# Performance work log

Measured on AMD Instinct MI355X. Metric: run time of the kernel, lower is better.

The kernel has to match this reference:

```python
import jax, jax.numpy as jnp
import numpy as np

CHUNK = 32
H = 4

def silu(x):
    return x * jax.nn.sigmoid(x)

def l2norm(x):
    return x * jax.lax.rsqrt(jnp.sum(x * x, -1, keepdims=True) + 1e-6)

def dwconv_causal(x_cl, w):
    # x_cl: (b, C, L), w: (C, k) depthwise causal conv (cross-correlation, left pad k-1)
    k = w.shape[1]
    xp = jnp.pad(x_cl, ((0, 0), (0, 0), (k - 1, 0)))
    return jax.lax.conv_general_dilated(xp, w[:, None, :], (1,), 'VALID',
        dimension_numbers=('NCH', 'OIH', 'NCH'), feature_group_count=x_cl.shape[1])

def short_conv_silu(x_bld, w):
    y = dwconv_causal(jnp.swapaxes(x_bld, 1, 2), w)
    return silu(jnp.swapaxes(y, 1, 2))

def delta_rule_chunkwise(q, k, v, beta, chunk=CHUNK):
    # q,k: (b,h,L,dk)  v: (b,h,L,dv)  beta: (b,h,L)
    b, h, L, dk = q.shape
    dv = v.shape[-1]
    pad = (-L) % chunk
    if pad:
        q, k, v = (jnp.pad(t, ((0, 0), (0, 0), (0, pad), (0, 0))) for t in (q, k, v))
        beta = jnp.pad(beta, ((0, 0), (0, 0), (0, pad)))
    n = (L + pad) // chunk
    q = l2norm(q)
    k = l2norm(k)
    v = v * beta[..., None]
    kb = k * beta[..., None]
    ch = lambda x: x.reshape(b, h, n, chunk, x.shape[-1])
    qc, kc, vc, kbc = map(ch, (q, k, v, kb))
    idx = jnp.arange(chunk)
    strict_lower = (idx[:, None] > idx[None, :]).astype(q.dtype)
    incl_lower = (idx[:, None] >= idx[None, :]).astype(q.dtype)
    # forward substitution to invert (I - tril(beta K K^T, -1)) per chunk
    attn = -jnp.einsum('bhncd,bhned->bhnce', kbc, kc) * strict_lower
    for i in range(1, chunk):
        upd = jnp.einsum('...j,...ji->...i', attn[..., i, :], attn[..., :, :i])
        attn = attn.at[..., i, :i].add(upd)
    attn = attn + jnp.eye(chunk, dtype=q.dtype)
    u = attn @ vc          # (b,h,n,c,dv)
    w = attn @ kbc         # (b,h,n,c,dk)
    xs = tuple(jnp.moveaxis(t, 2, 0) for t in (qc, kc, u, w))
    S0 = jnp.zeros((b, h, dk, dv), q.dtype)
    def step(S, x):
        qi, ki, ui, wi = x
        a_loc = jnp.einsum('bhcd,bhed->bhce', qi, ki) * incl_lower
        ui = ui - wi @ S
        oi = qi @ S + a_loc @ ui
        S = S + jnp.einsum('bhcd,bhcv->bhdv', ki, ui)
        return S, oi
    S, o = jax.lax.scan(step, S0, xs)
    o = jnp.moveaxis(o, 0, 2).reshape(b, h, n * chunk, dv)[:, :, :L]
    return o, S

def multiscale_conv(v, ms_w3, ms_w15, ms_w31, kernel_mix_w, channel_mixer_w):
    # v: (b,l,h,d)
    b, l, h, d = v.shape
    x = jnp.swapaxes(v.reshape(b, l, h * d), 1, 2)  # (b, h*d, l)
    outs = [dwconv_causal(x, w) for w in (ms_w3, ms_w15, ms_w31)]
    y = jnp.concatenate(outs, axis=1)               # (b, 3*h*d, l)
    # faithful to torch rearrange 'b (h kd) l -> b l h kd' on the concat layout
    y = y.reshape(b, h, 3 * d, l).transpose(0, 3, 1, 2)  # (b,l,h,3d)
    y = y @ kernel_mix_w                            # (b,l,h,d)
    y = (y.reshape(b, l, h * d) @ channel_mixer_w).reshape(b, l, h, d)
    return y

def _forward(hidden_states, Wq, Wk, Wv, Wb, conv_q_w, conv_k_w, conv_v_w,
             ms_w3, ms_w15, ms_w31, kernel_mix_w, channel_mixer_w,
             fusion_w1, fusion_b1, fusion_w2, fusion_b2, o_norm_w, Wo):
    b, L, D = hidden_states.shape
    h = H
    dk = Wq.shape[1] // h
    dv = Wv.shape[1] // h
    q = short_conv_silu(hidden_states @ Wq, conv_q_w).reshape(b, L, h, dk)
    k = short_conv_silu(hidden_states @ Wk, conv_k_w).reshape(b, L, h, dk)
    v = short_conv_silu(hidden_states @ Wv, conv_v_w).reshape(b, L, h, dv)
    v_direct = v
    beta = jax.nn.sigmoid(hidden_states @ Wb)  # (b,L,h)
    tr = lambda x: jnp.swapaxes(x, 1, 2)
    delta_out, _S = delta_rule_chunkwise(tr(q), tr(k), tr(v), tr(beta))
    delta_out = jnp.swapaxes(delta_out, 1, 2)  # (b,L,h,dv)
    ms_out = multiscale_conv(v_direct, ms_w3, ms_w15, ms_w31, kernel_mix_w, channel_mixer_w)
    bn = lambda x: jnp.mean(jnp.abs(x), -1)    # (b,L,h)
    gate_features = jnp.concatenate([hidden_states, bn(ms_out), bn(delta_out), bn(v_direct)], -1)
    hdn = jax.nn.gelu(gate_features @ fusion_w1 + fusion_b1, approximate=False)
    logits = (hdn @ fusion_w2 + fusion_b2).reshape(b, L, h, 3)
    wts = jax.nn.softmax(logits, -1)
    o = wts[..., 0:1] * ms_out + wts[..., 1:2] * delta_out + wts[..., 2:3] * v_direct
    o = o * jax.lax.rsqrt(jnp.mean(o * o, -1, keepdims=True) + 1e-5) * o_norm_w  # RMSNorm
    return o.reshape(b, L, h * dv) @ Wo

def setup_inputs() -> dict:
    B, L, D = 4, 2048, 1024
    h, d = H, D // H
    key = jax.random.key(0)
    ks = jax.random.split(key, 20)
    nrm = lambda k, shp, s: (jax.random.normal(k, shp, dtype=jnp.float32) * s)
    inp = {
        'hidden_states': nrm(ks[0], (B, L, D), 1.0),
        'Wq': nrm(ks[1], (D, D), D ** -0.5),
        'Wk': nrm(ks[2], (D, D), D ** -0.5),
        'Wv': nrm(ks[3], (D, D), D ** -0.5),
        'Wb': nrm(ks[4], (D, h), D ** -0.5),
        'conv_q_w': nrm(ks[5], (D, 4), 0.3),
        'conv_k_w': nrm(ks[6], (D, 4), 0.3),
        'conv_v_w': nrm(ks[7], (D, 4), 0.3),
        'ms_w3': nrm(ks[8], (D, 3), 0.02),
        'ms_w15': nrm(ks[9], (D, 15), 0.02),
        'ms_w31': nrm(ks[10], (D, 31), 0.02),
        'kernel_mix_w': nrm(ks[11], (3 * d, d), (3 * d) ** -0.5),
        'channel_mixer_w': nrm(ks[12], (D, D), D ** -0.5),
        'fusion_w1': nrm(ks[13], (D + 3 * h, 2 * D), (D + 3 * h) ** -0.5),
        'fusion_b1': jnp.zeros((2 * D,), jnp.float32),
        'fusion_w2': nrm(ks[14], (2 * D, 3 * h), (2 * D) ** -0.5),
        'fusion_b2': jnp.concatenate([jnp.zeros((2 * h,), jnp.float32), jnp.ones((h,), jnp.float32)]),
        'o_norm_w': jnp.ones((d,), jnp.float32),
        'Wo': nrm(ks[15], (D, D), D ** -0.5),
    }
    return inp

def reference(hidden_states, Wq, Wk, Wv, Wb, conv_q_w, conv_k_w, conv_v_w,
              ms_w3, ms_w15, ms_w31, kernel_mix_w, channel_mixer_w,
              fusion_w1, fusion_b1, fusion_w2, fusion_b2, o_norm_w, Wo):
    return _forward(hidden_states, Wq, Wk, Wv, Wb, conv_q_w, conv_k_w, conv_v_w,
                    ms_w3, ms_w15, ms_w31, kernel_mix_w, channel_mixer_w,
                    fusion_w1, fusion_b1, fusion_w2, fusion_b2, o_norm_w, Wo)
```

## Files before the change

### kernel.cpp

```cpp
#include <hip/hip_runtime.h>
#include <math.h>


typedef __attribute__((ext_vector_type(8))) __bf16 bf16x8;
typedef __attribute__((ext_vector_type(4))) float f32x4;

__device__ inline ushort f2bf(float f) {
    union { float f; unsigned u; } x; x.f = f;
    unsigned u = x.u;
    u += 0x7fffu + ((u >> 16) & 1u);
    return (ushort)(u >> 16);
}
__device__ inline float bf2f(ushort h) {
    union { unsigned u; float f; } x; x.u = ((unsigned)h) << 16;
    return x.f;
}
__device__ inline float ldf(float v) { return v; }
__device__ inline float ldf(ushort v) { return bf2f(v); }

template<int EPI>
__global__ __launch_bounds__(256) void gemm_mfma(
    const ushort* __restrict__ A, const ushort* __restrict__ BT,
    const float* __restrict__ bias, const float* __restrict__ extA,
    const float* __restrict__ extB, void* __restrict__ Cout,
    int M, int N, int K)
{
    __shared__ ushort As[2][128 * 32];
    __shared__ ushort Bs[2][128 * 32];
    __shared__ float bns[(EPI >= 2) ? 128 * 13 : 1];
    __shared__ float exb[(EPI >= 2) ? 12 * 128 : 1];
    const int tid = threadIdx.x;
    const int row0 = blockIdx.y * 128, col0 = blockIdx.x * 128;
    const int lane = tid & 63, wave = tid >> 6;
    const int wr = (wave >> 1) * 64, wc = (wave & 1) * 64;

    if (EPI >= 2) {
        for (int e = tid; e < 128 * 12; e += 256)
            bns[(e / 12) * 13 + (e % 12)] = extA[(long)(row0 + e / 12) * 12 + e % 12];
        for (int e = tid; e < 12 * 128; e += 256)
            exb[e] = extB[(long)(e >> 7) * N + col0 + (e & 127)];
    }

    f32x4 acc[4][4];
    #pragma unroll
    for (int m = 0; m < 4; ++m)
        #pragma unroll
        for (int n = 0; n < 4; ++n) {
            acc[m][n][0] = 0.f; acc[m][n][1] = 0.f;
            acc[m][n][2] = 0.f; acc[m][n][3] = 0.f;
        }

    const int rA = lane & 15;
    const int ko = (lane >> 4) * 8;
    const int srow = tid >> 2;
    const int skk = (tid & 3) * 8;

    for (int k0 = 0; k0 < K; k0 += 64) {
        #pragma unroll
        for (int hf = 0; hf < 2; ++hf) {
            #pragma unroll
            for (int i = 0; i < 2; ++i) {
                const long ga = (long)(row0 + i * 64 + srow) * K + k0 + hf * 32 + skk;
                __builtin_amdgcn_global_load_lds(
                    (const __attribute__((address_space(1))) void*)(A + ga),
                    (__attribute__((address_space(3))) void*)(&As[hf][0] + i * 2048 + wave * 512),
                    16, 0, 0);
                const long gb = (long)(col0 + i * 64 + srow) * K + k0 + hf * 32 + skk;
                __builtin_amdgcn_global_load_lds(
                    (const __attribute__((address_space(1))) void*)(BT + gb),
                    (__attribute__((address_space(3))) void*)(&Bs[hf][0] + i * 2048 + wave * 512),
                    16, 0, 0);
            }
        }
        __syncthreads();
        #pragma unroll
        for (int hf = 0; hf < 2; ++hf) {
            bf16x8 af[4], bfr[4];
            #pragma unroll
            for (int m = 0; m < 4; ++m)
                af[m] = *(const bf16x8*)(&As[hf][0] + (wr + m * 16 + rA) * 32 + ko);
            #pragma unroll
            for (int n = 0; n < 4; ++n)
                bfr[n] = *(const bf16x8*)(&Bs[hf][0] + (wc + n * 16 + rA) * 32 + ko);
            #pragma unroll
            for (int m = 0; m < 4; ++m)
                #pragma unroll
                for (int n = 0; n < 4; ++n)
                    acc[m][n] = __builtin_amdgcn_mfma_f32_16x16x32_bf16(af[m], bfr[n], acc[m][n], 0, 0, 0);
        }
        __syncthreads();
    }

    const int crow = (lane >> 4) * 4;
    const int ccol = lane & 15;
    #pragma unroll
    for (int m = 0; m < 4; ++m) {
        #pragma unroll
        for (int n = 0; n < 4; ++n) {
            #pragma unroll
            for (int r = 0; r < 4; ++r) {
                const int rl = wr + m * 16 + crow + r;
                const int cl = wc + n * 16 + ccol;
                float vv = acc[m][n][r];
                if (EPI >= 2) {
                    vv += bias[col0 + cl];
                    #pragma unroll
                    for (int j = 0; j < 12; ++j) vv += bns[rl * 13 + j] * exb[j * 128 + cl];
                    vv = 0.5f * vv * (1.f + erff(vv * 0.70710678118654752f));
                }
                const long off = (long)(row0 + rl) * N + col0 + cl;
                if (EPI == 0) ((float*)Cout)[off] = vv;
                else ((ushort*)Cout)[off] = f2bf(vv);
            }
        }
    }
}

__global__ __launch_bounds__(256) void transpose_cast(const float* __restrict__ W,
    ushort* __restrict__ WT, int K, int N)
{
    __shared__ float t[32][33];
    const int k0 = blockIdx.y * 32, n0 = blockIdx.x * 32;
    const int c = threadIdx.x & 31, r8 = threadIdx.x >> 5;
    #pragma unroll
    for (int rr = 0; rr < 4; ++rr) {
        const int r = r8 + rr * 8;
        t[r][c] = W[(long)(k0 + r) * N + n0 + c];
    }
    __syncthreads();
    #pragma unroll
    for (int rr = 0; rr < 4; ++rr) {
        const int r = r8 + rr * 8;
        WT[(long)(n0 + r) * K + k0 + c] = f2bf(t[c][r]);
    }
}

__global__ __launch_bounds__(256) void cast_bf16(const float* __restrict__ x,
    ushort* __restrict__ y)
{
    const long i = ((long)blockIdx.x * 256 + threadIdx.x) * 4;
    const float4 v = *(const float4*)(x + i);
    ushort4 o;
    o.x = f2bf(v.x); o.y = f2bf(v.y); o.z = f2bf(v.z); o.w = f2bf(v.w);
    *(ushort4*)(y + i) = o;
}

template<int NOUT, int MODE, typename TA>
__global__ __launch_bounds__(256) void gemm_smallN(const TA* __restrict__ A,
    const float* __restrict__ Bm, const float* __restrict__ bias,
    float* __restrict__ Cm, int K)
{
    __shared__ float part[4][NOUT];
    __shared__ float sm[NOUT];
    const int m = blockIdx.x, tid = threadIdx.x;
    const TA* ar = A + (long)m * K;
    float acc[NOUT];
    #pragma unroll
    for (int j = 0; j < NOUT; ++j) acc[j] = 0.f;
    for (int k = tid; k < K; k += 256) {
        const float a = ldf(ar[k]);
        #pragma unroll
        for (int j = 0; j < NOUT; ++j) acc[j] += a * Bm[(long)k * NOUT + j];
    }
    #pragma unroll
    for (int j = 0; j < NOUT; ++j)
        for (int off = 32; off > 0; off >>= 1) acc[j] += __shfl_down(acc[j], off);
    const int wid = tid >> 6, lane = tid & 63;
    if (lane == 0) {
        #pragma unroll
        for (int j = 0; j < NOUT; ++j) part[wid][j] = acc[j];
    }
    __syncthreads();
    if (tid < NOUT) {
        float s = part[0][tid] + part[1][tid] + part[2][tid] + part[3][tid];
        if (MODE == 0) {
            Cm[(long)m * NOUT + tid] = 1.f / (1.f + expf(-s));
        } else {
            sm[tid] = s + bias[tid];
        }
    }
    if (MODE == 1) {
        __syncthreads();
        if (tid < NOUT) {
            const int hh = tid / 3, r = tid - hh * 3;
            const float a0 = sm[hh * 3], a1 = sm[hh * 3 + 1], a2 = sm[hh * 3 + 2];
            const float mx = fmaxf(a0, fmaxf(a1, a2));
            const float e0 = expf(a0 - mx), e1 = expf(a1 - mx), e2 = expf(a2 - mx);
            const float mine = (r == 0) ? e0 : ((r == 1) ? e1 : e2);
            Cm[(long)m * NOUT + tid] = mine / (e0 + e1 + e2);
        }
    }
}

__global__ __launch_bounds__(256) void conv4_silu(const ushort* __restrict__ x,
    const float* __restrict__ wc, float* __restrict__ y)
{
    const long idx = (long)blockIdx.x * 256 + threadIdx.x;
    const int c = (int)(idx & 1023);
    const long bl = idx >> 10;
    const int l = (int)(bl & 2047);
    const ushort* xp = x + bl * 1024 + c;
    const float* wp = wc + c * 4;
    float s = 0.f;
    #pragma unroll
    for (int t = 0; t < 4; ++t) {
        const int ll = l - 3 + t;
        if (ll >= 0) s += bf2f(xp[(long)(ll - l) * 1024]) * wp[t];
    }
    y[idx] = s / (1.f + expf(-s));
}

__global__ __launch_bounds__(256) void conv4_silu_l2norm(const ushort* __restrict__ x,
    const float* __restrict__ wc, ushort* __restrict__ y)
{
    const int bl = blockIdx.x, tid = threadIdx.x;
    const int l = bl & 2047;
    const int c0 = tid * 4;
    const ushort* xp = x + (long)bl * 1024 + c0;
    float s[4] = {0.f, 0.f, 0.f, 0.f};
    #pragma unroll
    for (int t = 0; t < 4; ++t) {
        const int ll = l - 3 + t;
        if (ll >= 0) {
            const ushort4 xv = *(const ushort4*)(xp + (long)(ll - l) * 1024);
            s[0] += bf2f(xv.x) * wc[(c0 + 0) * 4 + t];
            s[1] += bf2f(xv.y) * wc[(c0 + 1) * 4 + t];
            s[2] += bf2f(xv.z) * wc[(c0 + 2) * 4 + t];
            s[3] += bf2f(xv.w) * wc[(c0 + 3) * 4 + t];
        }
    }
    #pragma unroll
    for (int i = 0; i < 4; ++i) s[i] = s[i] / (1.f + expf(-s[i]));
    float ss = s[0] * s[0] + s[1] * s[1] + s[2] * s[2] + s[3] * s[3];
    for (int off = 32; off > 0; off >>= 1) ss += __shfl_down(ss, off);
    ss = __shfl(ss, 0);
    const float inv = rsqrtf(ss + 1e-6f);
    ushort4 o;
    o.x = f2bf(s[0] * inv); o.y = f2bf(s[1] * inv);
    o.z = f2bf(s[2] * inv); o.w = f2bf(s[3] * inv);
    *(ushort4*)(y + (long)bl * 1024 + c0) = o;
}

__global__ __launch_bounds__(256) void chunk_prep(
    const ushort* __restrict__ qn, const ushort* __restrict__ kn,
    const float* __restrict__ v, const float* __restrict__ beta,
    float* __restrict__ u, ushort* __restrict__ w16,
    ushort* __restrict__ kT16, ushort* __restrict__ al16)
{
    __shared__ __align__(16) ushort kn16[32 * 264];
    __shared__ __align__(16) ushort kb16[32 * 264];
    __shared__ __align__(16) float  vb[32 * 260];
    __shared__ float Ms[32 * 33];
    __shared__ float Rs[32 * 33];
    __shared__ float bet[32];
    const int blk = blockIdx.x;
    const int n = blk & 63;
    const int bh = blk >> 6;
    const int h = bh & 3;
    const int b = bh >> 2;
    const int tid = threadIdx.x;
    const long lbase = (long)b * 2048 + n * 32;

    if (tid < 32) bet[tid] = beta[(lbase + tid) * 4 + h];
    __syncthreads();

    #pragma unroll
    for (int it = 0; it < 4; ++it) {
        const int e2 = tid + it * 256;
        const int c = e2 >> 5, d8 = (e2 & 31) * 8;
        const uint4 kv = *(const uint4*)(kn + (lbase + c) * 1024 + h * 256 + d8);
        *(uint4*)&kn16[c * 264 + d8] = kv;
        const float bc = bet[c];
        uint4 kb;
        kb.x = (uint)f2bf(bf2f((ushort)(kv.x & 0xffffu)) * bc) |
               ((uint)f2bf(bf2f((ushort)(kv.x >> 16)) * bc) << 16);
        kb.y = (uint)f2bf(bf2f((ushort)(kv.y & 0xffffu)) * bc) |
               ((uint)f2bf(bf2f((ushort)(kv.y >> 16)) * bc) << 16);
        kb.z = (uint)f2bf(bf2f((ushort)(kv.z & 0xffffu)) * bc) |
               ((uint)f2bf(bf2f((ushort)(kv.z >> 16)) * bc) << 16);
        kb.w = (uint)f2bf(bf2f((ushort)(kv.w & 0xffffu)) * bc) |
               ((uint)f2bf(bf2f((ushort)(kv.w >> 16)) * bc) << 16);
        *(uint4*)&kb16[c * 264 + d8] = kb;
    }
    #pragma unroll
    for (int it = 0; it < 8; ++it) {
        const int e2 = tid + it * 256;
        const int c = e2 >> 6, d4 = (e2 & 63) * 4;
        float4 vv = *(const float4*)(v + (lbase + c) * 1024 + h * 256 + d4);
        const float bc = bet[c];
        vv.x *= bc; vv.y *= bc; vv.z *= bc; vv.w *= bc;
        *(float4*)&vb[c * 260 + d4] = vv;
    }
    __syncthreads();

    for (int e = tid; e < 8192; e += 256)
        kT16[(long)blk * 8192 + e] = kn16[(e & 31) * 264 + (e >> 5)];

    const int lane = tid & 63, wave = tid >> 6;
    const int wr2 = (wave >> 1) * 16, wc2 = (wave & 1) * 16;
    const int rA = lane & 15, ko = (lane >> 4) * 8;
    {
        f32x4 accM, accA;
        accM[0] = 0.f; accM[1] = 0.f; accM[2] = 0.f; accM[3] = 0.f;
        accA[0] = 0.f; accA[1] = 0.f; accA[2] = 0.f; accA[3] = 0.f;
        const ushort* qrow = qn + (lbase + wr2 + rA) * 1024 + h * 256 + ko;
        #pragma unroll
        for (int ks = 0; ks < 8; ++ks) {
            const bf16x8 bfK = *(const bf16x8*)&kn16[(wc2 + rA) * 264 + ks * 32 + ko];
            const bf16x8 afM = *(const bf16x8*)&kb16[(wr2 + rA) * 264 + ks * 32 + ko];
            accM = __builtin_amdgcn_mfma_f32_16x16x32_bf16(afM, bfK, accM, 0, 0, 0);
            const bf16x8 afQ = *(const bf16x8*)(qrow + ks * 32);
            accA = __builtin_amdgcn_mfma_f32_16x16x32_bf16(afQ, bfK, accA, 0, 0, 0);
        }
        const int ccol = lane & 15, crow = (lane >> 4) * 4;
        #pragma unroll
        for (int r = 0; r < 4; ++r) {
            const int i = wr2 + crow + r, j = wc2 + ccol;
            const float mv = (i > j) ? -accM[r] : 0.f;
            Ms[i * 33 + j] = mv;
            Rs[i * 33 + j] = mv + ((i == j) ? 1.f : 0.f);
            al16[(long)blk * 1024 + i * 32 + j] = f2bf((i >= j) ? accA[r] : 0.f);
        }
    }
    __syncthreads();

    const int j = tid & 31, i0 = tid >> 5;
    for (int it = 0; it < 4; ++it) {
        float p4[4] = {0.f, 0.f, 0.f, 0.f};
        for (int kk = 0; kk < 32; ++kk) {
            const float pb = Ms[kk * 33 + j];
            #pragma unroll
            for (int ii = 0; ii < 4; ++ii) p4[ii] += Ms[(i0 + 8 * ii) * 33 + kk] * pb;
        }
        __syncthreads();
        #pragma unroll
        for (int ii = 0; ii < 4; ++ii) Ms[(i0 + 8 * ii) * 33 + j] = p4[ii];
        __syncthreads();
        float r4[4] = {0.f, 0.f, 0.f, 0.f};
        for (int kk = 0; kk < 32; ++kk) {
            const float pb = Ms[kk * 33 + j];
            #pragma unroll
            for (int ii = 0; ii < 4; ++ii) r4[ii] += Rs[(i0 + 8 * ii) * 33 + kk] * pb;
        }
        __syncthreads();
        #pragma unroll
        for (int ii = 0; ii < 4; ++ii) Rs[(i0 + 8 * ii) * 33 + j] += r4[ii];
        __syncthreads();
    }

    {
        const int dd = tid;
        float accU[32], accW[32];
        #pragma unroll
        for (int r = 0; r < 32; ++r) { accU[r] = 0.f; accW[r] = 0.f; }
        for (int kk = 0; kk < 32; ++kk) {
            const float vv = vb[kk * 260 + dd];
            const float bb = bf2f(kb16[kk * 264 + dd]);
            #pragma unroll
            for (int r = 0; r < 32; ++r) {
                const float rr = Rs[r * 33 + kk];
                accU[r] += rr * vv;
                accW[r] += rr * bb;
            }
        }
        const long base = (long)blk * 32;
        #pragma unroll
        for (int r = 0; r < 32; ++r) {
            u  [(base + r) * 256 + dd] = accU[r];
            w16[(base + r) * 256 + dd] = f2bf(accW[r]);
        }
    }
}

__global__ __launch_bounds__(64, 1) void delta_scan_mfma(
    const ushort* __restrict__ q16, const ushort* __restrict__ kT16,
    const ushort* __restrict__ w16, const float* __restrict__ u,
    const ushort* __restrict__ al16, float* __restrict__ dt)
{
    __shared__ __align__(16) ushort Sb[16 * 264];
    __shared__ __align__(16) ushort Ub[16 * 40];
    const int blk = blockIdx.x;
    const int bh = blk & 15;
    const int sl = blk >> 4;
    const int h = bh & 3;
    const int b = bh >> 2;
    const int v0 = sl * 16;
    const int lane = threadIdx.x;
    const int col = lane & 15;
    const int grp = lane >> 4;

    const ushort* wp  = w16  + ((long)bh * 64 * 32 + col) * 256 + grp * 8;
    const ushort* qp  = q16  + ((long)b * 2048 + col) * 1024 + h * 256 + grp * 8;
    const ushort* kp  = kT16 + ((long)bh * 64 * 256 + col) * 32 + grp * 8;
    const ushort* ap  = al16 + ((long)bh * 64 * 32 + col) * 32 + grp * 8;
    const float*  Ug  = u    + ((long)bh * 64 * 32 + grp * 4) * 256 + v0 + col;
    float*        dp  = dt   + ((long)b * 2048 + grp * 4) * 1024 + h * 256 + v0 + col;

    f32x4 S[16];
    #pragma unroll
    for (int t = 0; t < 16; ++t) { S[t][0] = 0.f; S[t][1] = 0.f; S[t][2] = 0.f; S[t][3] = 0.f; }

    bf16x8 wf[2][8], qf[2][8], kf[16], alf[2], sf[8];
    float upre[8];

    #pragma unroll
    for (int kb = 0; kb < 8; ++kb)
        #pragma unroll
        for (int e = 0; e < 8; ++e) sf[kb][e] = (__bf16)0.f;

    #pragma unroll
    for (int rt = 0; rt < 2; ++rt)
        #pragma unroll
        for (int kb = 0; kb < 8; ++kb) {
            wf[rt][kb] = *(const bf16x8*)(wp + rt * 4096 + kb * 32);
            qf[rt][kb] = *(const bf16x8*)(qp + (long)rt * 16384 + kb * 32);
        }
    #pragma unroll
    for (int t = 0; t < 16; ++t) kf[t] = *(const bf16x8*)(kp + t * 512);
    alf[0] = *(const bf16x8*)(ap);
    alf[1] = *(const bf16x8*)(ap + 512);
    #pragma unroll
    for (int rt = 0; rt < 2; ++rt)
        #pragma unroll
        for (int r = 0; r < 4; ++r)
            upre[rt * 4 + r] = Ug[rt * 4096 + r * 256];

    for (int n = 0; n < 64; ++n) {
        f32x4 up[2];
        #pragma unroll
        for (int rt = 0; rt < 2; ++rt) {
            f32x4 a; a[0] = 0.f; a[1] = 0.f; a[2] = 0.f; a[3] = 0.f;
            #pragma unroll
            for (int kb = 0; kb < 8; ++kb)
                a = __builtin_amdgcn_mfma_f32_16x16x32_bf16(wf[rt][kb], sf[kb], a, 0, 0, 0);
            #pragma unroll
            for (int r = 0; r < 4; ++r)
                up[rt][r] = upre[rt * 4 + r] - a[r];
        }
        if (n < 63) {
            #pragma unroll
            for (int rt = 0; rt < 2; ++rt)
                #pragma unroll
                for (int kb = 0; kb < 8; ++kb)
                    wf[rt][kb] = *(const bf16x8*)(wp + (long)(n + 1) * 8192 + rt * 4096 + kb * 32);
        }

        #pragma unroll
        for (int rt = 0; rt < 2; ++rt) {
            ushort4 p;
            p.x = f2bf(up[rt][0]); p.y = f2bf(up[rt][1]);
            p.z = f2bf(up[rt][2]); p.w = f2bf(up[rt][3]);
            *(ushort4*)&Ub[col * 40 + rt * 16 + grp * 4] = p;
        }
        const bf16x8 uf = *(const bf16x8*)&Ub[col * 40 + grp * 8];

        #pragma unroll
        for (int rt = 0; rt < 2; ++rt) {
            f32x4 a; a[0] = 0.f; a[1] = 0.f; a[2] = 0.f; a[3] = 0.f;
            #pragma unroll
            for (int kb = 0; kb < 8; ++kb)
                a = __builtin_amdgcn_mfma_f32_16x16x32_bf16(qf[rt][kb], sf[kb], a, 0, 0, 0);
            a = __builtin_amdgcn_mfma_f32_16x16x32_bf16(alf[rt], uf, a, 0, 0, 0);
            #pragma unroll
            for (int r = 0; r < 4; ++r)
                dp[(long)n * 32768 + rt * 16384 + r * 1024] = a[r];
        }
        if (n < 63) {
            #pragma unroll
            for (int rt = 0; rt < 2; ++rt)
                #pragma unroll
                for (int kb = 0; kb < 8; ++kb)
                    qf[rt][kb] = *(const bf16x8*)(qp + (long)(n + 1) * 32768 + (long)rt * 16384 + kb * 32);
            alf[0] = *(const bf16x8*)(ap + (long)(n + 1) * 1024);
            alf[1] = *(const bf16x8*)(ap + (long)(n + 1) * 1024 + 512);
        }

        #pragma unroll
        for (int t = 0; t < 16; ++t)
            S[t] = __builtin_amdgcn_mfma_f32_16x16x32_bf16(kf[t], uf, S[t], 0, 0, 0);
        if (n < 63) {
            #pragma unroll
            for (int t = 0; t < 16; ++t)
                kf[t] = *(const bf16x8*)(kp + (long)(n + 1) * 8192 + t * 512);
            #pragma unroll
            for (int rt = 0; rt < 2; ++rt)
                #pragma unroll
                for (int r = 0; r < 4; ++r)
                    upre[rt * 4 + r] = Ug[(long)(n + 1) * 8192 + rt * 4096 + r * 256];
        }

        #pragma unroll
        for (int t = 0; t < 16; ++t) {
            ushort4 p;
            p.x = f2bf(S[t][0]); p.y = f2bf(S[t][1]);
            p.z = f2bf(S[t][2]); p.w = f2bf(S[t][3]);
            *(ushort4*)&Sb[col * 264 + t * 16 + grp * 4] = p;
        }
        #pragma unroll
        for (int kb = 0; kb < 8; ++kb)
            sf[kb] = *(const bf16x8*)&Sb[col * 264 + kb * 32 + grp * 8];
    }
}

__global__ __launch_bounds__(256) void ms_conv(const float* __restrict__ v,
    const float* __restrict__ w3, const float* __restrict__ w15,
    const float* __restrict__ w31, ushort* __restrict__ y)
{
    const int bid = blockIdx.x;
    const int b = bid >> 10;
    const int oct = (bid >> 2) & 255;
    const int c = ((bid & 3) << 8) + threadIdx.x;
    const int l0 = oct << 3;
    const float* vb = v + ((long)b * 2048) * 1024 + c;
    ushort* yb = y + ((long)b * 2048) * 3072 + c;

    float win[38];
    #pragma unroll
    for (int t = 0; t < 38; ++t) {
        const int ll = l0 - 30 + t;
        win[t] = (ll >= 0) ? vb[(long)ll * 1024] : 0.f;
    }
    {
        float W[31];
        #pragma unroll
        for (int t = 0; t < 31; ++t) W[t] = w31[c * 31 + t];
        #pragma unroll
        for (int j = 0; j < 8; ++j) {
            float s = 0.f;
            #pragma unroll
            for (int t = 0; t < 31; ++t) s += win[j + t] * W[t];
            yb[(long)(l0 + j) * 3072 + 2048] = f2bf(s);
        }
    }
    {
        float W[15];
        #pragma unroll
        for (int t = 0; t < 15; ++t) W[t] = w15[c * 15 + t];
        #pragma unroll
        for (int j = 0; j < 8; ++j) {
            float s = 0.f;
            #pragma unroll
            for (int t = 0; t < 15; ++t) s += win[j + 16 + t] * W[t];
            yb[(long)(l0 + j) * 3072 + 1024] = f2bf(s);
        }
    }
    {
        float W[3];
        #pragma unroll
        for (int t = 0; t < 3; ++t) W[t] = w3[c * 3 + t];
        #pragma unroll
        for (int j = 0; j < 8; ++j) {
            float s = 0.f;
            #pragma unroll
            for (int t = 0; t < 3; ++t) s += win[j + 28 + t] * W[t];
            yb[(long)(l0 + j) * 3072] = f2bf(s);
        }
    }
}

__global__ __launch_bounds__(256) void build_bn(const ushort* __restrict__ ms,
    const float* __restrict__ dt, const float* __restrict__ v,
    float* __restrict__ bn)
{
    const int bl = blockIdx.x, tid = threadIdx.x;
    const long rb = (long)bl * 1024;
    const int wid = tid >> 6, lane = tid & 63;
    const long base = rb + wid * 256 + lane * 4;
    float* g = bn + (long)bl * 12;
    float s;

    const ushort4 mu = *(const ushort4*)(ms + base);
    s = fabsf(bf2f(mu.x)) + fabsf(bf2f(mu.y)) + fabsf(bf2f(mu.z)) + fabsf(bf2f(mu.w));
    for (int off = 32; off > 0; off >>= 1) s += __shfl_down(s, off);
    if (lane == 0) g[wid] = s * (1.f / 256.f);

    const float4 d = *(const float4*)(dt + base);
    s = fabsf(d.x) + fabsf(d.y) + fabsf(d.z) + fabsf(d.w);
    for (int off = 32; off > 0; off >>= 1) s += __shfl_down(s, off);
    if (lane == 0) g[4 + wid] = s * (1.f / 256.f);

    const float4 a = *(const float4*)(v + base);
    s = fabsf(a.x) + fabsf(a.y) + fabsf(a.z) + fabsf(a.w);
    for (int off = 32; off > 0; off >>= 1) s += __shfl_down(s, off);
    if (lane == 0) g[8 + wid] = s * (1.f / 256.f);
}

__global__ __launch_bounds__(256) void blend_rms(const ushort* __restrict__ ms,
    const float* __restrict__ dt, const float* __restrict__ v,
    const float* __restrict__ wts, const float* __restrict__ onw,
    ushort* __restrict__ o)
{
    const int bl = blockIdx.x, tid = threadIdx.x;
    const int wid = tid >> 6, lane = tid & 63;
    const long base = (long)bl * 1024 + wid * 256 + lane * 4;
    const float* wr = wts + (long)bl * 12 + wid * 3;
    const float w0 = wr[0], w1 = wr[1], w2 = wr[2];
    const ushort4 mu = *(const ushort4*)(ms + base);
    const float4 d = *(const float4*)(dt + base);
    const float4 x = *(const float4*)(v + base);
    float4 ov;
    ov.x = w0 * bf2f(mu.x) + w1 * d.x + w2 * x.x;
    ov.y = w0 * bf2f(mu.y) + w1 * d.y + w2 * x.y;
    ov.z = w0 * bf2f(mu.z) + w1 * d.z + w2 * x.z;
    ov.w = w0 * bf2f(mu.w) + w1 * d.w + w2 * x.w;
    float ss = ov.x * ov.x + ov.y * ov.y + ov.z * ov.z + ov.w * ov.w;
    for (int off = 32; off > 0; off >>= 1) ss += __shfl_down(ss, off);
    ss = __shfl(ss, 0);
    const float inv = rsqrtf(ss * (1.f / 256.f) + 1e-5f);
    const float4 nw = *(const float4*)(onw + lane * 4);
    ushort4 ob;
    ob.x = f2bf(ov.x * inv * nw.x); ob.y = f2bf(ov.y * inv * nw.y);
    ob.z = f2bf(ov.z * inv * nw.z); ob.w = f2bf(ov.w * inv * nw.w);
    *(ushort4*)(o + base) = ob;
}

extern "C" void kernel_launch(void* const* d_in, const int* in_sizes, int n_in,
                              void* d_out, int out_size, void* d_ws, size_t ws_size,
                              hipStream_t stream)
{
    (void)in_sizes; (void)n_in; (void)out_size; (void)ws_size;
    const float* hid   = (const float*)d_in[0];
    const float* Wq    = (const float*)d_in[1];
    const float* Wk    = (const float*)d_in[2];
    const float* Wv    = (const float*)d_in[3];
    const float* Wb    = (const float*)d_in[4];
    const float* cq    = (const float*)d_in[5];
    const float* ck    = (const float*)d_in[6];
    const float* cv    = (const float*)d_in[7];
    const float* w3    = (const float*)d_in[8];
    const float* w15   = (const float*)d_in[9];
    const float* w31   = (const float*)d_in[10];
    const float* kmix  = (const float*)d_in[11];
    const float* cmix  = (const float*)d_in[12];
    const float* fw1   = (const float*)d_in[13];
    const float* fb1   = (const float*)d_in[14];
    const float* fw2   = (const float*)d_in[15];
    const float* fb2   = (const float*)d_in[16];
    const float* onw   = (const float*)d_in[17];
    const float* Wo    = (const float*)d_in[18];
    float* out = (float*)d_out;

    const size_t MiB = 1024 * 1024;
    char* W = (char*)d_ws;
    float*  s0    = (float*)(W);
    char*   s1c   = W + 32 * MiB;
    float*  s2    = (float*)(W + 64 * MiB);
    char*   s3    = W + 96 * MiB;
    float*  s4    = (float*)(W + 128 * MiB);
    ushort* hid16 = (ushort*)(W + 160 * MiB);
    ushort* WqT   = (ushort*)(W + 176 * MiB);
    ushort* WkT   = WqT   + 1024 * 1024;
    ushort* WvT   = WkT   + 1024 * 1024;
    ushort* cmixT = WvT   + 1024 * 1024;
    ushort* WoT   = cmixT + 1024 * 1024;
    ushort* fw1T  = WoT   + 1024 * 1024;
    ushort* kmixT = fw1T  + 2048 * 1024;
    float*  beta  = (float*)(W + 191 * MiB);
    ushort* al16  = (ushort*)(W + 191 * MiB + 128 * 1024);
    float*  bnf   = (float*)(W + 193 * MiB + 128 * 1024);
    float*  wts   = bnf + 98304;

    ushort* q16    = (ushort*)s3;
    ushort* k16    = (ushort*)(s3 + 16 * MiB);
    ushort* mix16  = q16;
    ushort* ofin16 = k16;
    ushort* yms16  = (ushort*)s0;
    ushort* hdn16  = (ushort*)s0;
    ushort* qkvlin16 = (ushort*)s0;
    float*  u = s0;
    ushort* w16  = (ushort*)s1c;
    ushort* kT16 = (ushort*)(s1c + 16 * MiB);
    float*  dt = s2;
    float*  v = s4;
    ushort* msout16 = (ushort*)s1c;

    const dim3 T256(256);
    cast_bf16<<<8192, T256, 0, stream>>>(hid, hid16);
    transpose_cast<<<dim3(32, 32), T256, 0, stream>>>(Wq, WqT, 1024, 1024);
    transpose_cast<<<dim3(32, 32), T256, 0, stream>>>(Wk, WkT, 1024, 1024);
    transpose_cast<<<dim3(32, 32), T256, 0, stream>>>(Wv, WvT, 1024, 1024);
    transpose_cast<<<dim3(32, 32), T256, 0, stream>>>(cmix, cmixT, 1024, 1024);
    transpose_cast<<<dim3(32, 32), T256, 0, stream>>>(Wo, WoT, 1024, 1024);
    transpose_cast<<<dim3(64, 32), T256, 0, stream>>>(fw1, fw1T, 1024, 2048);
    transpose_cast<<<dim3(8, 24), T256, 0, stream>>>(kmix, kmixT, 768, 256);
    gemm_mfma<1><<<dim3(8, 64), T256, 0, stream>>>(hid16, WqT, nullptr, nullptr, nullptr, qkvlin16, 8192, 1024, 1024);
    conv4_silu_l2norm<<<8192, T256, 0, stream>>>(qkvlin16, cq, q16);
    gemm_mfma<1><<<dim3(8, 64), T256, 0, stream>>>(hid16, WkT, nullptr, nullptr, nullptr, qkvlin16, 8192, 1024, 1024);
    conv4_silu_l2norm<<<8192, T256, 0, stream>>>(qkvlin16, ck, k16);
    gemm_mfma<1><<<dim3(8, 64), T256, 0, stream>>>(hid16, WvT, nullptr, nullptr, nullptr, qkvlin16, 8192, 1024, 1024);
    conv4_silu<<<32768, T256, 0, stream>>>(qkvlin16, cv, v);
    gemm_smallN<4, 0><<<8192, T256, 0, stream>>>(hid16, Wb, nullptr, beta, 1024);
    chunk_prep<<<1024, T256, 0, stream>>>(q16, k16, v, beta, u, w16, kT16, al16);
    delta_scan_mfma<<<256, dim3(64), 0, stream>>>(q16, kT16, w16, u, al16, dt);
    ms_conv<<<4096, T256, 0, stream>>>(v, w3, w15, w31, yms16);
    gemm_mfma<1><<<dim3(2, 256), T256, 0, stream>>>(yms16, kmixT, nullptr, nullptr, nullptr, mix16, 32768, 256, 768);
    gemm_mfma<1><<<dim3(8, 64), T256, 0, stream>>>(mix16, cmixT, nullptr, nullptr, nullptr, msout16, 8192, 1024, 1024);
    build_bn<<<8192, T256, 0, stream>>>(msout16, dt, v, bnf);
    gemm_mfma<3><<<dim3(16, 64), T256, 0, stream>>>(hid16, fw1T, fb1, bnf, fw1 + 1024L * 2048, hdn16, 8192, 2048, 1024);
    gemm_smallN<12, 1><<<8192, T256, 0, stream>>>(hdn16, fw2, fb2, wts, 2048);
    blend_rms<<<8192, T256, 0, stream>>>(msout16, dt, v, wts, onw, ofin16);
    gemm_mfma<0><<<dim3(8, 64), T256, 0, stream>>>(ofin16, WoT, nullptr, nullptr, nullptr, out, 8192, 1024, 1024);
}
```

Measured before the change: 746.0 us.

## Store v, u, dt in bf16 and co-schedule ms_conv blocks with delta scan

The intermediates v, u and the delta-rule output dt are now stored as bf16 instead of fp32, roughly halving their write and read traffic across chunk_prep, the scan, build_bn and blend_rms. The separate multiscale conv kernel is merged into the delta-scan launch as extra 64-thread blocks past index 256. Those blocks can fill the GPU while the 256 latency-bound serial scan blocks run. This lowers the precision of these intermediates, which risks accuracy, and changes the conv block shape to 64 threads.

```diff
diff --git a/kernel.cpp b/kernel.cpp
--- a/kernel.cpp
+++ b/kernel.cpp
@@ -193,7 +193,7 @@
 }
 
 __global__ __launch_bounds__(256) void conv4_silu(const ushort* __restrict__ x,
-    const float* __restrict__ wc, float* __restrict__ y)
+    const float* __restrict__ wc, ushort* __restrict__ y)
 {
     const long idx = (long)blockIdx.x * 256 + threadIdx.x;
     const int c = (int)(idx & 1023);
@@ -207,7 +207,7 @@
         const int ll = l - 3 + t;
         if (ll >= 0) s += bf2f(xp[(long)(ll - l) * 1024]) * wp[t];
     }
-    y[idx] = s / (1.f + expf(-s));
+    y[idx] = f2bf(s / (1.f + expf(-s)));
 }
 
 __global__ __launch_bounds__(256) void conv4_silu_l2norm(const ushort* __restrict__ x,
@@ -243,8 +243,8 @@
 
 __global__ __launch_bounds__(256) void chunk_prep(
     const ushort* __restrict__ qn, const ushort* __restrict__ kn,
-    const float* __restrict__ v, const float* __restrict__ beta,
-    float* __restrict__ u, ushort* __restrict__ w16,
+    const ushort* __restrict__ v16, const float* __restrict__ beta,
+    ushort* __restrict__ u16, ushort* __restrict__ w16,
     ushort* __restrict__ kT16, ushort* __restrict__ al16)
 {
     __shared__ __align__(16) ushort kn16[32 * 264];
@@ -286,10 +286,12 @@
     for (int it = 0; it < 8; ++it) {
         const int e2 = tid + it * 256;
         const int c = e2 >> 6, d4 = (e2 & 63) * 4;
-        float4 vv = *(const float4*)(v + (lbase + c) * 1024 + h * 256 + d4);
+        const ushort4 vv = *(const ushort4*)(v16 + (lbase + c) * 1024 + h * 256 + d4);
         const float bc = bet[c];
-        vv.x *= bc; vv.y *= bc; vv.z *= bc; vv.w *= bc;
-        *(float4*)&vb[c * 260 + d4] = vv;
+        float4 vf;
+        vf.x = bf2f(vv.x) * bc; vf.y = bf2f(vv.y) * bc;
+        vf.z = bf2f(vv.z) * bc; vf.w = bf2f(vv.w) * bc;
+        *(float4*)&vb[c * 260 + d4] = vf;
     }
     __syncthreads();
 
@@ -366,17 +368,75 @@
         const long base = (long)blk * 32;
         #pragma unroll
         for (int r = 0; r < 32; ++r) {
-            u  [(base + r) * 256 + dd] = accU[r];
+            u16[(base + r) * 256 + dd] = f2bf(accU[r]);
             w16[(base + r) * 256 + dd] = f2bf(accW[r]);
         }
     }
 }
 
-__global__ __launch_bounds__(64, 1) void delta_scan_mfma(
+__global__ __launch_bounds__(64, 1) void delta_scan_msconv(
     const ushort* __restrict__ q16, const ushort* __restrict__ kT16,
-    const ushort* __restrict__ w16, const float* __restrict__ u,
-    const ushort* __restrict__ al16, float* __restrict__ dt)
-{
+    const ushort* __restrict__ w16, const ushort* __restrict__ u16,
+    const ushort* __restrict__ al16, ushort* __restrict__ dt,
+    const ushort* __restrict__ v16, const float* __restrict__ w3,
+    const float* __restrict__ w15, const float* __restrict__ w31,
+    ushort* __restrict__ yms)
+{
+    if (blockIdx.x >= 256) {
+        const int cid = blockIdx.x - 256;
+        const int b = cid >> 12;
+        const int rem = cid & 4095;
+        const int oct = rem >> 4;
+        const int c = ((rem & 15) << 6) + (int)threadIdx.x;
+        const int l0 = oct << 3;
+        const ushort* vp = v16 + ((long)b * 2048) * 1024 + c;
+        ushort* yb = yms + ((long)b * 2048) * 3072 + c;
+
+        float win[38];
+        #pragma unroll
+        for (int t = 0; t < 38; ++t) {
+            const int ll = l0 - 30 + t;
+            win[t] = (ll >= 0) ? bf2f(vp[(long)ll * 1024]) : 0.f;
+        }
+        {
+            float Wt[31];
+            #pragma unroll
+            for (int t = 0; t < 31; ++t) Wt[t] = w31[c * 31 + t];
+            #pragma unroll
+            for (int j = 0; j < 8; ++j) {
+                float s = 0.f;
+                #pragma unroll
+                for (int t = 0; t < 31; ++t) s += win[j + t] * Wt[t];
+                yb[(long)(l0 + j) * 3072 + 2048] = f2bf(s);
+            }
+        }
+        {
+            float Wt[15];
+            #pragma unroll
+            for (int t = 0; t < 15; ++t) Wt[t] = w15[c * 15 + t];
+            #pragma unroll
+            for (int j = 0; j < 8; ++j) {
+                float s = 0.f;
+                #pragma unroll
+                for (int t = 0; t < 15; ++t) s += win[j + 16 + t] * Wt[t];
+                yb[(long)(l0 + j) * 3072 + 1024] = f2bf(s);
+            }
+        }
+        {
+            float Wt[3];
+            #pragma unroll
+            for (int t = 0; t < 3; ++t) Wt[t] = w3[c * 3 + t];
+            #pragma unroll
+            for (int j = 0; j < 8; ++j) {
+                float s = 0.f;
+                #pragma unroll
+                for (int t = 0; t < 3; ++t) s += win[j + 28 + t] * Wt[t];
+                yb[(long)(l0 + j) * 3072] = f2bf(s);
+            }
+        }
+        return;
+    }
+
     __shared__ __align__(16) ushort Sb[16 * 264];
     __shared__ __align__(16) ushort Ub[16 * 40];
     const int blk = blockIdx.x;
@@ -393,8 +453,8 @@
     const ushort* qp  = q16  + ((long)b * 2048 + col) * 1024 + h * 256 + grp * 8;
     const ushort* kp  = kT16 + ((long)bh * 64 * 256 + col) * 32 + grp * 8;
     const ushort* ap  = al16 + ((long)bh * 64 * 32 + col) * 32 + grp * 8;
-    const float*  Ug  = u    + ((long)bh * 64 * 32 + grp * 4) * 256 + v0 + col;
-    float*        dp  = dt   + ((long)b * 2048 + grp * 4) * 1024 + h * 256 + v0 + col;
+    const ushort* Ug  = u16  + ((long)bh * 64 * 32 + grp * 4) * 256 + v0 + col;
+    ushort*       dp  = dt   + ((long)b * 2048 + grp * 4) * 1024 + h * 256 + v0 + col;
 
     f32x4 S[16];
     #pragma unroll
@@ -423,7 +483,7 @@
     for (int rt = 0; rt < 2; ++rt)
         #pragma unroll
         for (int r = 0; r < 4; ++r)
-            upre[rt * 4 + r] = Ug[rt * 4096 + r * 256];
+            upre[rt * 4 + r] = bf2f(Ug[rt * 4096 + r * 256]);
 
     for (int n = 0; n < 64; ++n) {
         f32x4 up[2];
@@ -463,7 +523,7 @@
             a = __builtin_amdgcn_mfma_f32_16x16x32_bf16(alf[rt], uf, a, 0, 0, 0);
             #pragma unroll
             for (int r = 0; r < 4; ++r)
-                dp[(long)n * 32768 + rt * 16384 + r * 1024] = a[r];
+                dp[(long)n * 32768 + rt * 16384 + r * 1024] = f2bf(a[r]);
         }
         if (n < 63) {
             #pragma unroll
@@ -486,7 +546,7 @@
             for (int rt = 0; rt < 2; ++rt)
                 #pragma unroll
                 for (int r = 0; r < 4; ++r)
-                    upre[rt * 4 + r] = Ug[(long)(n + 1) * 8192 + rt * 4096 + r * 256];
+                    upre[rt * 4 + r] = bf2f(Ug[(long)(n + 1) * 8192 + rt * 4096 + r * 256]);
         }
 
         #pragma unroll
@@ -502,64 +562,8 @@
     }
 }
 
-__global__ __launch_bounds__(256) void ms_conv(const float* __restrict__ v,
-    const float* __restrict__ w3, const float* __restrict__ w15,
-    const float* __restrict__ w31, ushort* __restrict__ y)
-{
-    const int bid = blockIdx.x;
-    const int b = bid >> 10;
-    const int oct = (bid >> 2) & 255;
-    const int c = ((bid & 3) << 8) + threadIdx.x;
-    const int l0 = oct << 3;
-    const float* vb = v + ((long)b * 2048) * 1024 + c;
-    ushort* yb = y + ((long)b * 2048) * 3072 + c;
-
-    float win[38];
-    #pragma unroll
-    for (int t = 0; t < 38; ++t) {
-        const int ll = l0 - 30 + t;
-        win[t] = (ll >= 0) ? vb[(long)ll * 1024] : 0.f;
-    }
-    {
-        float W[31];
-        #pragma unroll
-        for (int t = 0; t < 31; ++t) W[t] = w31[c * 31 + t];
-        #pragma unroll
-        for (int j = 0; j < 8; ++j) {
-            float s = 0.f;
-            #pragma unroll
-            for (int t = 0; t < 31; ++t) s += win[j + t] * W[t];
-            yb[(long)(l0 + j) * 3072 + 2048] = f2bf(s);
-        }
-    }
-    {
-        float W[15];
-        #pragma unroll
-        for (int t = 0; t < 15; ++t) W[t] = w15[c * 15 + t];
-        #pragma unroll
-        for (int j = 0; j < 8; ++j) {
-            float s = 0.f;
-            #pragma unroll
-            for (int t = 0; t < 15; ++t) s += win[j + 16 + t] * W[t];
-            yb[(long)(l0 + j) * 3072 + 1024] = f2bf(s);
-        }
-    }
-    {
-        float W[3];
-        #pragma unroll
-        for (int t = 0; t < 3; ++t) W[t] = w3[c * 3 + t];
-        #pragma unroll
-        for (int j = 0; j < 8; ++j) {
-            float s = 0.f;
-            #pragma unroll
-            for (int t = 0; t < 3; ++t) s += win[j + 28 + t] * W[t];
-            yb[(long)(l0 + j) * 3072] = f2bf(s);
-        }
-    }
-}
-
 __global__ __launch_bounds__(256) void build_bn(const ushort* __restrict__ ms,
-    const float* __restrict__ dt, const float* __restrict__ v,
+    const ushort* __restrict__ dt, const ushort* __restrict__ v,
     float* __restrict__ bn)
 {
     const int bl = blockIdx.x, tid = threadIdx.x;
@@ -574,19 +578,19 @@
     for (int off = 32; off > 0; off >>= 1) s += __shfl_down(s, off);
     if (lane == 0) g[wid] = s * (1.f / 256.f);
 
-    const float4 d = *(const float4*)(dt + base);
-    s = fabsf(d.x) + fabsf(d.y) + fabsf(d.z) + fabsf(d.w);
+    const ushort4 du = *(const ushort4*)(dt + base);
+    s = fabsf(bf2f(du.x)) + fabsf(bf2f(du.y)) + fabsf(bf2f(du.z)) + fabsf(bf2f(du.w));
     for (int off = 32; off > 0; off >>= 1) s += __shfl_down(s, off);
     if (lane == 0) g[4 + wid] = s * (1.f / 256.f);
 
-    const float4 a = *(const float4*)(v + base);
-    s = fabsf(a.x) + fabsf(a.y) + fabsf(a.z) + fabsf(a.w);
+    const ushort4 vu = *(const ushort4*)(v + base);
+    s = fabsf(bf2f(vu.x)) + fabsf(bf2f(vu.y)) + fabsf(bf2f(vu.z)) + fabsf(bf2f(vu.w));
     for (int off = 32; off > 0; off >>= 1) s += __shfl_down(s, off);
     if (lane == 0) g[8 + wid] = s * (1.f / 256.f);
 }
 
 __global__ __launch_bounds__(256) void blend_rms(const ushort* __restrict__ ms,
-    const float* __restrict__ dt, const float* __restrict__ v,
+    const ushort* __restrict__ dt, const ushort* __restrict__ v,
     const float* __restrict__ wts, const float* __restrict__ onw,
     ushort* __restrict__ o)
 {
@@ -596,13 +600,13 @@
     const float* wr = wts + (long)bl * 12 + wid * 3;
     const float w0 = wr[0], w1 = wr[1], w2 = wr[2];
     const ushort4 mu = *(const ushort4*)(ms + base);
-    const float4 d = *(const float4*)(dt + base);
-    const float4 x = *(const float4*)(v + base);
+    const ushort4 du = *(const ushort4*)(dt + base);
+    const ushort4 vu = *(const ushort4*)(v + base);
     float4 ov;
-    ov.x = w0 * bf2f(mu.x) + w1 * d.x + w2 * x.x;
-    ov.y = w0 * bf2f(mu.y) + w1 * d.y + w2 * x.y;
-    ov.z = w0 * bf2f(mu.z) + w1 * d.z + w2 * x.z;
-    ov.w = w0 * bf2f(mu.w) + w1 * d.w + w2 * x.w;
+    ov.x = w0 * bf2f(mu.x) + w1 * bf2f(du.x) + w2 * bf2f(vu.x);
+    ov.y = w0 * bf2f(mu.y) + w1 * bf2f(du.y) + w2 * bf2f(vu.y);
+    ov.z = w0 * bf2f(mu.z) + w1 * bf2f(du.z) + w2 * bf2f(vu.z);
+    ov.w = w0 * bf2f(mu.w) + w1 * bf2f(du.w) + w2 * bf2f(vu.w);
     float ss = ov.x * ov.x + ov.y * ov.y + ov.z * ov.z + ov.w * ov.w;
     for (int off = 32; off > 0; off >>= 1) ss += __shfl_down(ss, off);
     ss = __shfl(ss, 0);
@@ -642,37 +646,32 @@
 
     const size_t MiB = 1024 * 1024;
     char* W = (char*)d_ws;
-    float*  s0    = (float*)(W);
-    char*   s1c   = W + 32 * MiB;
-    float*  s2    = (float*)(W + 64 * MiB);
-    char*   s3    = W + 96 * MiB;
-    float*  s4    = (float*)(W + 128 * MiB);
-    ushort* hid16 = (ushort*)(W + 160 * MiB);
-    ushort* WqT   = (ushort*)(W + 176 * MiB);
-    ushort* WkT   = WqT   + 1024 * 1024;
-    ushort* WvT   = WkT   + 1024 * 1024;
-    ushort* cmixT = WvT   + 1024 * 1024;
-    ushort* WoT   = cmixT + 1024 * 1024;
-    ushort* fw1T  = WoT   + 1024 * 1024;
-    ushort* kmixT = fw1T  + 2048 * 1024;
-    float*  beta  = (float*)(W + 191 * MiB);
-    ushort* al16  = (ushort*)(W + 191 * MiB + 128 * 1024);
-    float*  bnf   = (float*)(W + 193 * MiB + 128 * 1024);
-    float*  wts   = bnf + 98304;
-
-    ushort* q16    = (ushort*)s3;
-    ushort* k16    = (ushort*)(s3 + 16 * MiB);
-    ushort* mix16  = q16;
-    ushort* ofin16 = k16;
-    ushort* yms16  = (ushort*)s0;
-    ushort* hdn16  = (ushort*)s0;
-    ushort* qkvlin16 = (ushort*)s0;
-    float*  u = s0;
-    ushort* w16  = (ushort*)s1c;
-    ushort* kT16 = (ushort*)(s1c + 16 * MiB);
-    float*  dt = s2;
-    float*  v = s4;
-    ushort* msout16 = (ushort*)s1c;
+    ushort* yms16    = (ushort*)W;
+    ushort* qkvlin16 = (ushort*)W;
+    ushort* q16  = (ushort*)(W + 48 * MiB);
+    ushort* k16  = (ushort*)(W + 64 * MiB);
+    ushort* w16  = (ushort*)(W + 80 * MiB);
+    ushort* kT16 = (ushort*)(W + 96 * MiB);
+    ushort* u16  = (ushort*)(W + 112 * MiB);
+    ushort* dt16 = (ushort*)(W + 128 * MiB);
+    ushort* v16  = (ushort*)(W + 144 * MiB);
+    ushort* hid16= (ushort*)(W + 160 * MiB);
+    ushort* WqT  = (ushort*)(W + 176 * MiB);
+    ushort* WkT  = WqT   + 1024 * 1024;
+    ushort* WvT  = WkT   + 1024 * 1024;
+    ushort* cmixT= WvT   + 1024 * 1024;
+    ushort* WoT  = cmixT + 1024 * 1024;
+    ushort* fw1T = WoT   + 1024 * 1024;
+    ushort* kmixT= fw1T  + 2048 * 1024;
+    float*  beta = (float*)(W + 191 * MiB);
+    ushort* al16 = (ushort*)(W + 191 * MiB + 128 * 1024);
+    float*  bnf  = (float*)(W + 193 * MiB + 128 * 1024);
+    float*  wts  = bnf + 98304;
+
+    ushort* hdn16   = q16;
+    ushort* mix16   = k16;
+    ushort* msout16 = w16;
+    ushort* ofin16  = kT16;
 
     const dim3 T256(256);
     cast_bf16<<<8192, T256, 0, stream>>>(hid, hid16);
@@ -688,16 +687,16 @@
     gemm_mfma<1><<<dim3(8, 64), T256, 0, stream>>>(hid16, WkT, nullptr, nullptr, nullptr, qkvlin16, 8192, 1024, 1024);
     conv4_silu_l2norm<<<8192, T256, 0, stream>>>(qkvlin16, ck, k16);
     gemm_mfma<1><<<dim3(8, 64), T256, 0, stream>>>(hid16, WvT, nullptr, nullptr, nullptr, qkvlin16, 8192, 1024, 1024);
-    conv4_silu<<<32768, T256, 0, stream>>>(qkvlin16, cv, v);
+    conv4_silu<<<32768, T256, 0, stream>>>(qkvlin16, cv, v16);
     gemm_smallN<4, 0><<<8192, T256, 0, stream>>>(hid16, Wb, nullptr, beta, 1024);
-    chunk_prep<<<1024, T256, 0, stream>>>(q16, k16, v, beta, u, w16, kT16, al16);
-    delta_scan_mfma<<<256, dim3(64), 0, stream>>>(q16, kT16, w16, u, al16, dt);
-    ms_conv<<<4096, T256, 0, stream>>>(v, w3, w15, w31, yms16);
+    chunk_prep<<<1024, T256, 0, stream>>>(q16, k16, v16, beta, u16, w16, kT16, al16);
+    delta_scan_msconv<<<16640, dim3(64), 0, stream>>>(q16, kT16, w16, u16, al16, dt16,
+                                                      v16, w3, w15, w31, yms16);
     gemm_mfma<1><<<dim3(2, 256), T256, 0, stream>>>(yms16, kmixT, nullptr, nullptr, nullptr, mix16, 32768, 256, 768);
     gemm_mfma<1><<<dim3(8, 64), T256, 0, stream>>>(mix16, cmixT, nullptr, nullptr, nullptr, msout16, 8192, 1024, 1024);
-    build_bn<<<8192, T256, 0, stream>>>(msout16, dt, v, bnf);
+    build_bn<<<8192, T256, 0, stream>>>(msout16, dt16, v16, bnf);
     gemm_mfma<3><<<dim3(16, 64), T256, 0, stream>>>(hid16, fw1T, fb1, bnf, fw1 + 1024L * 2048, hdn16, 8192, 2048, 1024);
     gemm_smallN<12, 1><<<8192, T256, 0, stream>>>(hdn16, fw2, fb2, wts, 2048);
-    blend_rms<<<8192, T256, 0, stream>>>(msout16, dt, v, wts, onw, ofin16);
+    blend_rms<<<8192, T256, 0, stream>>>(msout16, dt16, v16, wts, onw, ofin16);
     gemm_mfma<0><<<dim3(8, 64), T256, 0, stream>>>(ofin16, WoT, nullptr, nullptr, nullptr, out, 8192, 1024, 1024);
 }
```

Measured after the change: 772.4 us. 3.5% more time.
